# Kernel optimization log

Measured on AMD Instinct MI355X. Metric: run time of the kernel, lower is better.

## Reference

```python
import jax, jax.numpy as jnp
import numpy as np

B, S, HID = 4, 2048, 2048
NH, NKV, HD = 16, 4, 128
GROUPS = NH // NKV
THETA = 10000.0
SCALING = 1.0
SCALE = HD ** -0.5


def setup_inputs() -> dict:
    key = jax.random.key(0)
    k1, k2, k3 = jax.random.split(key, 3)
    hidden_states = jax.random.normal(k1, (B, S, HID), dtype=jnp.float32)
    # stored as [in, out] so x @ W matches torch Linear(x) with W = weight.T
    W_qkv = jax.random.normal(k2, (HID, (NH + 2 * NKV) * HD), dtype=jnp.float32) * (HID ** -0.5)
    W_o = jax.random.normal(k3, (HID, HID), dtype=jnp.float32) * (HID ** -0.5)
    return {"hidden_states": hidden_states, "W_qkv": W_qkv, "W_o": W_o}


def _rope_tables(seq_len, dtype):
    inv_freq = 1.0 / (THETA ** (jnp.arange(0, HD, 2, dtype=jnp.float32) / HD))
    t = jnp.arange(seq_len, dtype=jnp.float32) / SCALING
    freqs = jnp.einsum("s,d->sd", t, inv_freq)          # [S, HD/2]
    emb = jnp.concatenate([freqs, freqs], axis=-1)        # [S, HD]
    return jnp.cos(emb).astype(dtype), jnp.sin(emb).astype(dtype)


def _rotate_half(x):
    x1, x2 = jnp.split(x, 2, axis=-1)
    return jnp.concatenate([-x2, x1], axis=-1)


def _apply_rope(x, cos, sin):
    # x: [B, H, S, D]; cos/sin: [S, D]
    return x * cos[None, None] + _rotate_half(x) * sin[None, None]


def reference(hidden_states, W_qkv, W_o):
    b, s, _ = hidden_states.shape
    qkv = hidden_states @ W_qkv                           # [B, S, (NH+2NKV)*HD]
    q, k, v = jnp.split(qkv, [NH * HD, (NH + NKV) * HD], axis=-1)
    q = q.reshape(b, s, NH, HD).transpose(0, 2, 1, 3)      # [B, NH, S, D]
    k = k.reshape(b, s, NKV, HD).transpose(0, 2, 1, 3)     # [B, NKV, S, D]
    v = v.reshape(b, s, NKV, HD).transpose(0, 2, 1, 3)

    cos, sin = _rope_tables(s, hidden_states.dtype)
    q = _apply_rope(q, cos, sin)
    k = _apply_rope(k, cos, sin)

    # GQA attention without materializing expanded K/V
    qg = q.reshape(b, NKV, GROUPS, s, HD)                  # [B, NKV, G, Sq, D]
    scores = jnp.einsum("bkgqd,bkKd->bkgqK", qg, k) * SCALE
    causal = jnp.tril(jnp.ones((s, s), dtype=bool))
    scores = jnp.where(causal[None, None, None], scores, jnp.finfo(scores.dtype).min)
    probs = jax.nn.softmax(scores, axis=-1)
    out = jnp.einsum("bkgqK,bkKd->bkgqd", probs, v)        # [B, NKV, G, Sq, D]
    out = out.reshape(b, NH, s, HD).transpose(0, 2, 1, 3).reshape(b, s, HID)
    return out @ W_o
```

## Files before the change

kernel.cpp:

```cpp
#include <hip/hip_runtime.h>

#define B_ 4
#define S_ 2048
#define HID_ 2048
#define NH_ 16
#define NKV_ 4
#define HD_ 128
#define NTOK (B_ * S_)
#define QKV_N 3072
#define KO_N 512
#define SCALE_ 0.08838834764831845f
#define NEG_ -30000.0f

typedef __attribute__((ext_vector_type(8))) short short8;
typedef __attribute__((ext_vector_type(4))) short short4v;
typedef __attribute__((ext_vector_type(4))) float f32x4;
typedef unsigned short ushort_t;
typedef unsigned int uint32;

__device__ __forceinline__ float sanit(float x) {
    if (!(x == x)) x = 0.0f;
    return fminf(fmaxf(x, -65504.0f), 65504.0f);
}
__device__ __forceinline__ ushort_t f2bf(float f) {
    union { float f; uint32 u; } c; c.f = f;
    uint32 u = c.u;
    u += 0x7fffu + ((u >> 16) & 1u);
    return (ushort_t)(u >> 16);
}
__device__ __forceinline__ ushort_t f2bf_s(float f) { return f2bf(sanit(f)); }
__device__ __forceinline__ float bf2f(ushort_t h) {
    union { float f; uint32 u; } c; c.u = ((uint32)h) << 16;
    return c.f;
}

__device__ __forceinline__ void gl16(const ushort_t* g, ushort_t* l) {
    __builtin_amdgcn_global_load_lds(
        (__attribute__((address_space(1))) void*)g,
        (__attribute__((address_space(3))) void*)l, 16, 0, 0);
}

__global__ void convx_kernel(const float* __restrict__ X, ushort_t* __restrict__ Xb) {
    size_t i = (size_t)blockIdx.x * blockDim.x + threadIdx.x;
    const float4 a = *(const float4*)(X + i * 8);
    const float4 b = *(const float4*)(X + i * 8 + 4);
    short8 p;
    p[0] = (short)f2bf(a.x); p[1] = (short)f2bf(a.y);
    p[2] = (short)f2bf(a.z); p[3] = (short)f2bf(a.w);
    p[4] = (short)f2bf(b.x); p[5] = (short)f2bf(b.y);
    p[6] = (short)f2bf(b.z); p[7] = (short)f2bf(b.w);
    *(short8*)(Xb + i * 8) = p;
}

__global__ void wtrans_kernel(const float* __restrict__ W, ushort_t* __restrict__ Wt,
                              int K, int N) {
    __shared__ float tile[32][33];
    const int n0 = blockIdx.x * 32;
    const int k0 = blockIdx.y * 32;
    const int t  = threadIdx.x;
    const int r  = t >> 3;
    const int c  = (t & 7) * 4;
    const float4 v = *(const float4*)(W + (size_t)(k0 + r) * N + n0 + c);
    tile[r][c] = v.x; tile[r][c + 1] = v.y; tile[r][c + 2] = v.z; tile[r][c + 3] = v.w;
    __syncthreads();
    short4v p;
    p[0] = (short)f2bf(tile[c][r]);
    p[1] = (short)f2bf(tile[c + 1][r]);
    p[2] = (short)f2bf(tile[c + 2][r]);
    p[3] = (short)f2bf(tile[c + 3][r]);
    *(short4v*)(Wt + (size_t)(n0 + r) * K + k0 + c) = p;
}

template <int SPLIT>
__global__ __launch_bounds__(256, 2) void gemm_bt(
    const ushort_t* __restrict__ A, const ushort_t* __restrict__ Bt,
    void* __restrict__ C0, ushort_t* __restrict__ C1, ushort_t* __restrict__ C2,
    int M, int N, int K) {
    __shared__ __align__(16) ushort_t As[128 * 32];
    __shared__ __align__(16) ushort_t Bs[128 * 32];

    const int tid  = threadIdx.x;
    const int lane = tid & 63;
    const int w    = tid >> 6;
    const int wm   = (w >> 1) * 64;
    const int wn   = (w & 1) * 64;
    const int m0   = blockIdx.y * 128;
    const int n0   = blockIdx.x * 128;
    const int col  = lane & 15;
    const int quad = lane >> 4;

    f32x4 acc[4][4] = {};

    const int sr = tid >> 2;
    const int sk = (tid & 3) * 8;
    const ushort_t* ag0 = A + (size_t)(m0 + sr) * K + sk;
    const ushort_t* ag1 = A + (size_t)(m0 + 64 + sr) * K + sk;
    const ushort_t* bg0 = Bt + (size_t)(n0 + sr) * K + sk;
    const ushort_t* bg1 = Bt + (size_t)(n0 + 64 + sr) * K + sk;
    ushort_t* la0 = &As[tid * 8];
    ushort_t* la1 = &As[2048 + tid * 8];
    ushort_t* lb0 = &Bs[tid * 8];
    ushort_t* lb1 = &Bs[2048 + tid * 8];

    for (int k0 = 0; k0 < K; k0 += 32) {
        __syncthreads();
        gl16(ag0 + k0, la0);
        gl16(ag1 + k0, la1);
        gl16(bg0 + k0, lb0);
        gl16(bg1 + k0, lb1);
        __syncthreads();

        short8 af[4], bfr[4];
#pragma unroll
        for (int mt = 0; mt < 4; ++mt)
            af[mt] = *(const short8*)&As[(wm + mt * 16 + col) * 32 + quad * 8];
#pragma unroll
        for (int nt = 0; nt < 4; ++nt)
            bfr[nt] = *(const short8*)&Bs[(wn + nt * 16 + col) * 32 + quad * 8];
#pragma unroll
        for (int mt = 0; mt < 4; ++mt)
#pragma unroll
            for (int nt = 0; nt < 4; ++nt)
                acc[mt][nt] = __builtin_amdgcn_mfma_f32_16x16x32_bf16(
                    af[mt], bfr[nt], acc[mt][nt], 0, 0, 0);
    }

    if (SPLIT) {
        if (n0 >= 2560) {
#pragma unroll
            for (int mt = 0; mt < 4; ++mt)
#pragma unroll
                for (int nt = 0; nt < 4; ++nt) {
                    int cc   = n0 + wn + nt * 16 + col - 2560;
                    int row0 = m0 + wm + mt * 16 + quad * 4;
                    short4v p;
#pragma unroll
                    for (int r = 0; r < 4; ++r) p[r] = (short)f2bf_s(acc[mt][nt][r]);
                    *(short4v*)&C2[(size_t)cc * NTOK + row0] = p;
                }
        } else {
            ushort_t* dst;
            int ldc, coff;
            if (n0 >= 2048) { dst = C1; ldc = KO_N; coff = 2048; }
            else            { dst = (ushort_t*)C0; ldc = HID_; coff = 0; }
#pragma unroll
            for (int mt = 0; mt < 4; ++mt)
#pragma unroll
                for (int nt = 0; nt < 4; ++nt)
#pragma unroll
                    for (int r = 0; r < 4; ++r) {
                        int row = m0 + wm + mt * 16 + quad * 4 + r;
                        int cc  = n0 + wn + nt * 16 + col - coff;
                        dst[(size_t)row * ldc + cc] = f2bf_s(acc[mt][nt][r]);
                    }
        }
    } else {
        float* dst = (float*)C0;
#pragma unroll
        for (int mt = 0; mt < 4; ++mt)
#pragma unroll
            for (int nt = 0; nt < 4; ++nt)
#pragma unroll
                for (int r = 0; r < 4; ++r) {
                    int row = m0 + wm + mt * 16 + quad * 4 + r;
                    int cc  = n0 + wn + nt * 16 + col;
                    dst[(size_t)row * N + cc] = sanit(acc[mt][nt][r]);
                }
    }
}

__global__ void rope_kernel(ushort_t* __restrict__ qbuf,
                            ushort_t* __restrict__ kb) {
    int p = blockIdx.x * blockDim.x + threadIdx.x;
    const int total = NTOK * 20 * 64;
    if (p >= total) return;
    int d    = p & 63;
    int rest = p >> 6;
    int head = rest % 20;
    int tok  = rest / 20;
    int s    = tok & (S_ - 1);

    ushort_t* base;
    if (head < 16) base = qbuf + (size_t)tok * HID_ + head * HD_ + d;
    else           base = kb   + (size_t)tok * KO_N + (head - 16) * HD_ + d;

    float x1 = bf2f(base[0]);
    float x2 = bf2f(base[64]);

    float inv_freq = powf(10000.0f, -(float)d * (1.0f / 64.0f));
    float ang = (float)s * inv_freq;
    float sn, cs;
    sincosf(ang, &sn, &cs);

    base[0]  = f2bf_s(x1 * cs - x2 * sn);
    base[64] = f2bf_s(x2 * cs + x1 * sn);
}

__global__ __launch_bounds__(512, 4) void flash_kernel(
    const ushort_t* __restrict__ qbuf, const ushort_t* __restrict__ kb,
    const ushort_t* __restrict__ vtg, ushort_t* __restrict__ obuf) {
    __shared__ __align__(16) ushort_t Ks[64][136];
    __shared__ __align__(16) ushort_t Vt[128][72];
    __shared__ __align__(16) ushort_t Ps[8][16][72];

    const int tid  = threadIdx.x;
    const int lane = tid & 63;
    const int w    = tid >> 6;
    const int col  = lane & 15;
    const int quad = lane >> 4;
    const int q0   = (S_ / 128 - 1 - blockIdx.x) * 128;
    const int h    = blockIdx.y;
    const int b    = blockIdx.z;
    const int kvh  = h >> 2;
    const int bS   = b * S_;

    const int wr    = q0 + w * 16;
    const int wmax  = wr + 15;
    const int i_row = wr + quad * 4;

    short8 qf[4];
    {
        const ushort_t* qp = qbuf + (size_t)(bS + wr + col) * HID_
                             + h * HD_ + quad * 8;
#pragma unroll
        for (int kt = 0; kt < 4; ++kt) qf[kt] = *(const short8*)(qp + kt * 32);
    }

    float m_i[4], l_i[4];
#pragma unroll
    for (int r = 0; r < 4; ++r) { m_i[r] = NEG_; l_i[r] = 0.f; }
    f32x4 o[8] = {};

    const int ntiles = q0 / 64 + 2;

    const int jr = tid >> 3;
    const int kd = (tid & 7) * 16;
    const int vd = tid >> 2;
    const int vj = (tid & 3) * 16;

    const ushort_t* kgb = kb + (size_t)(bS + jr) * KO_N + kvh * HD_ + kd;
    const ushort_t* vgb = vtg + (size_t)(kvh * HD_ + vd) * NTOK + bS + vj;

    float4 pk0, pk1, pv0, pv1;
    pk0 = *(const float4*)(kgb);
    pk1 = *(const float4*)(kgb + 8);
    pv0 = *(const float4*)(vgb);
    pv1 = *(const float4*)(vgb + 8);
    *(float4*)&Ks[jr][kd]     = pk0;
    *(float4*)&Ks[jr][kd + 8] = pk1;
    *(float4*)&Vt[vd][vj]     = pv0;
    *(float4*)&Vt[vd][vj + 8] = pv1;
    __syncthreads();

    for (int t = 0; t < ntiles; ++t) {
        const int j0 = t * 64;
        const bool pre = (t + 1 < ntiles);
        if (pre) {
            const ushort_t* kgn = kgb + (size_t)(j0 + 64) * KO_N;
            const ushort_t* vgn = vgb + (j0 + 64);
            pk0 = *(const float4*)(kgn);
            pk1 = *(const float4*)(kgn + 8);
            pv0 = *(const float4*)(vgn);
            pv1 = *(const float4*)(vgn + 8);
        }

        if (j0 <= wmax) {
            f32x4 s[4] = {};
#pragma unroll
            for (int ct = 0; ct < 4; ++ct)
#pragma unroll
                for (int kt = 0; kt < 4; ++kt) {
                    short8 kf = *(const short8*)&Ks[ct * 16 + col][kt * 32 + quad * 8];
                    s[ct] = __builtin_amdgcn_mfma_f32_16x16x32_bf16(qf[kt], kf, s[ct], 0, 0, 0);
                }

            if (j0 + 64 > wr) {
#pragma unroll
                for (int ct = 0; ct < 4; ++ct) {
                    int jg = j0 + ct * 16 + col;
#pragma unroll
                    for (int r = 0; r < 4; ++r)
                        s[ct][r] = (jg > i_row + r) ? NEG_ : s[ct][r] * SCALE_;
                }
            } else {
#pragma unroll
                for (int ct = 0; ct < 4; ++ct)
#pragma unroll
                    for (int r = 0; r < 4; ++r) s[ct][r] *= SCALE_;
            }

            float mx[4];
#pragma unroll
            for (int r = 0; r < 4; ++r) {
                float m = fmaxf(fmaxf(s[0][r], s[1][r]), fmaxf(s[2][r], s[3][r]));
#pragma unroll
                for (int off = 1; off < 16; off <<= 1)
                    m = fmaxf(m, __shfl_xor(m, off, 64));
                mx[r] = m;
            }
            int ok = 1;
#pragma unroll
            for (int r = 0; r < 4; ++r) ok &= (mx[r] <= m_i[r] + 8.0f) ? 1 : 0;
            if (!__all(ok)) {
#pragma unroll
                for (int r = 0; r < 4; ++r) {
                    float mn = fmaxf(m_i[r], mx[r]);
                    float a  = __expf(m_i[r] - mn);
                    m_i[r] = mn;
                    l_i[r] *= a;
#pragma unroll
                    for (int dt = 0; dt < 8; ++dt) o[dt][r] *= a;
                }
            }
#pragma unroll
            for (int r = 0; r < 4; ++r) {
                float sum = 0.f;
#pragma unroll
                for (int ct = 0; ct < 4; ++ct) {
                    float p = __expf(s[ct][r] - m_i[r]);
                    s[ct][r] = p;
                    sum += p;
                }
#pragma unroll
                for (int off = 1; off < 16; off <<= 1)
                    sum += __shfl_xor(sum, off, 64);
                l_i[r] += sum;
            }

#pragma unroll
            for (int ct = 0; ct < 4; ++ct)
#pragma unroll
                for (int r = 0; r < 4; ++r)
                    Ps[w][quad * 4 + r][ct * 16 + col] = f2bf(s[ct][r]);

#pragma unroll
            for (int kt = 0; kt < 2; ++kt) {
                short8 pf = *(const short8*)&Ps[w][col][kt * 32 + quad * 8];
#pragma unroll
                for (int dt = 0; dt < 8; ++dt) {
                    short8 vf = *(const short8*)&Vt[dt * 16 + col][kt * 32 + quad * 8];
                    o[dt] = __builtin_amdgcn_mfma_f32_16x16x32_bf16(pf, vf, o[dt], 0, 0, 0);
                }
            }
        }

        __syncthreads();
        if (pre) {
            *(float4*)&Ks[jr][kd]     = pk0;
            *(float4*)&Ks[jr][kd + 8] = pk1;
            *(float4*)&Vt[vd][vj]     = pv0;
            *(float4*)&Vt[vd][vj + 8] = pv1;
            __syncthreads();
        }
    }

#pragma unroll
    for (int r = 0; r < 4; ++r) {
        float inv = 1.0f / fmaxf(l_i[r], 1e-30f);
        ushort_t* op = obuf + (size_t)(bS + i_row + r) * HID_ + h * HD_;
#pragma unroll
        for (int dt = 0; dt < 8; ++dt)
            op[dt * 16 + col] = f2bf_s(o[dt][r] * inv);
    }
}

extern "C" void kernel_launch(void* const* d_in, const int* in_sizes, int n_in,
                              void* d_out, int out_size, void* d_ws, size_t ws_size,
                              hipStream_t stream) {
    const float* X    = (const float*)d_in[0];
    const float* Wqkv = (const float*)d_in[1];
    const float* Wo   = (const float*)d_in[2];

    ushort_t* qb  = (ushort_t*)d_out;
    ushort_t* xh  = (ushort_t*)d_out + (size_t)NTOK * HID_;
    ushort_t* kb  = (ushort_t*)d_ws;
    ushort_t* vtg = kb + (size_t)NTOK * KO_N;
    ushort_t* wqt = vtg + (size_t)NTOK * KO_N;
    ushort_t* wot = (ushort_t*)d_ws + (size_t)NTOK * HID_;
    ushort_t* oa  = (ushort_t*)d_ws;

    convx_kernel<<<NTOK * HID_ / (256 * 8), 256, 0, stream>>>(X, xh);
    wtrans_kernel<<<dim3(QKV_N / 32, HID_ / 32), 256, 0, stream>>>(Wqkv, wqt, HID_, QKV_N);
    wtrans_kernel<<<dim3(HID_ / 32, HID_ / 32), 256, 0, stream>>>(Wo, wot, HID_, HID_);
    gemm_bt<1><<<dim3(QKV_N / 128, NTOK / 128), 256, 0, stream>>>(
        xh, wqt, qb, kb, vtg, NTOK, QKV_N, HID_);
    rope_kernel<<<(NTOK * 20 * 64) / 256, 256, 0, stream>>>(qb, kb);
    flash_kernel<<<dim3(S_ / 128, NH_, B_), 512, 0, stream>>>(qb, kb, vtg, xh);
    hipMemcpyAsync(oa, xh, (size_t)NTOK * HID_ * sizeof(ushort_t),
                   hipMemcpyDeviceToDevice, stream);
    gemm_bt<0><<<dim3(HID_ / 128, NTOK / 128), 256, 0, stream>>>(
        oa, wot, d_out, nullptr, nullptr, NTOK, HID_, HID_);
}
```

Measured before the change: 675.3 us.

## Load K/V fragments directly from global memory in flash kernel, drop LDS staging

Rewrites the flash attention kernel so each wave reads its K and V^T MFMA fragments straight from global memory (relying on cache) instead of staging shared tiles in LDS with block-wide barriers. Block size halves to 256 threads covering 64 query rows, doubling the grid, and each wave runs its own causal trip count, so there are no idle tiles or __syncthreads. It also adds s_setprio around the MFMA groups and splits the PV loads into two halves. The cost is redundant global/L2 traffic, since four waves and the four heads sharing a KV head each re-read the same K/V, plus less regular access patterns.

```diff
diff --git a/kernel.cpp b/kernel.cpp
--- a/kernel.cpp
+++ b/kernel.cpp
@@ -196,26 +196,23 @@
     base[64] = f2bf_s(x2 * cs + x1 * sn);
 }
 
-__global__ __launch_bounds__(512, 4) void flash_kernel(
+__global__ __launch_bounds__(256, 4) void flash_kernel(
     const ushort_t* __restrict__ qbuf, const ushort_t* __restrict__ kb,
     const ushort_t* __restrict__ vtg, ushort_t* __restrict__ obuf) {
-    __shared__ __align__(16) ushort_t Ks[64][136];
-    __shared__ __align__(16) ushort_t Vt[128][72];
-    __shared__ __align__(16) ushort_t Ps[8][16][72];
+    __shared__ __align__(16) ushort_t Ps[4][16][72];
 
     const int tid  = threadIdx.x;
     const int lane = tid & 63;
     const int w    = tid >> 6;
     const int col  = lane & 15;
     const int quad = lane >> 4;
-    const int q0   = (S_ / 128 - 1 - blockIdx.x) * 128;
+    const int q0   = (S_ / 64 - 1 - blockIdx.x) * 64;
     const int h    = blockIdx.y;
     const int b    = blockIdx.z;
     const int kvh  = h >> 2;
     const int bS   = b * S_;
 
     const int wr    = q0 + w * 16;
-    const int wmax  = wr + 15;
     const int i_row = wr + quad * 4;
 
     short8 qf[4];
@@ -231,126 +228,115 @@
     for (int r = 0; r < 4; ++r) { m_i[r] = NEG_; l_i[r] = 0.f; }
     f32x4 o[8] = {};
 
-    const int ntiles = q0 / 64 + 2;
-
-    const int jr = tid >> 3;
-    const int kd = (tid & 7) * 16;
-    const int vd = tid >> 2;
-    const int vj = (tid & 3) * 16;
-
-    const ushort_t* kgb = kb + (size_t)(bS + jr) * KO_N + kvh * HD_ + kd;
-    const ushort_t* vgb = vtg + (size_t)(kvh * HD_ + vd) * NTOK + bS + vj;
-
-    float4 pk0, pk1, pv0, pv1;
-    pk0 = *(const float4*)(kgb);
-    pk1 = *(const float4*)(kgb + 8);
-    pv0 = *(const float4*)(vgb);
-    pv1 = *(const float4*)(vgb + 8);
-    *(float4*)&Ks[jr][kd]     = pk0;
-    *(float4*)&Ks[jr][kd + 8] = pk1;
-    *(float4*)&Vt[vd][vj]     = pv0;
-    *(float4*)&Vt[vd][vj + 8] = pv1;
-    __syncthreads();
-
-    for (int t = 0; t < ntiles; ++t) {
+    const int nt = wr / 64 + 1;
+
+    const ushort_t* kbase = kb + (size_t)bS * KO_N + (size_t)kvh * HD_;
+    const ushort_t* vbase = vtg + (size_t)kvh * HD_ * NTOK + bS;
+
+    for (int t = 0; t < nt; ++t) {
         const int j0 = t * 64;
-        const bool pre = (t + 1 < ntiles);
-        if (pre) {
-            const ushort_t* kgn = kgb + (size_t)(j0 + 64) * KO_N;
-            const ushort_t* vgn = vgb + (j0 + 64);
-            pk0 = *(const float4*)(kgn);
-            pk1 = *(const float4*)(kgn + 8);
-            pv0 = *(const float4*)(vgn);
-            pv1 = *(const float4*)(vgn + 8);
-        }
-
-        if (j0 <= wmax) {
-            f32x4 s[4] = {};
+
+        f32x4 s[4] = {};
+#pragma unroll
+        for (int ct = 0; ct < 4; ++ct) {
+            const ushort_t* kr = kbase + (size_t)(j0 + ct * 16 + col) * KO_N + quad * 8;
+            short8 kf0 = *(const short8*)(kr);
+            short8 kf1 = *(const short8*)(kr + 32);
+            short8 kf2 = *(const short8*)(kr + 64);
+            short8 kf3 = *(const short8*)(kr + 96);
+            __builtin_amdgcn_s_setprio(1);
+            s[ct] = __builtin_amdgcn_mfma_f32_16x16x32_bf16(qf[0], kf0, s[ct], 0, 0, 0);
+            s[ct] = __builtin_amdgcn_mfma_f32_16x16x32_bf16(qf[1], kf1, s[ct], 0, 0, 0);
+            s[ct] = __builtin_amdgcn_mfma_f32_16x16x32_bf16(qf[2], kf2, s[ct], 0, 0, 0);
+            s[ct] = __builtin_amdgcn_mfma_f32_16x16x32_bf16(qf[3], kf3, s[ct], 0, 0, 0);
+            __builtin_amdgcn_s_setprio(0);
+        }
+
+        short8 vf0[8];
+#pragma unroll
+        for (int dt = 0; dt < 8; ++dt)
+            vf0[dt] = *(const short8*)(vbase + (size_t)(dt * 16 + col) * NTOK
+                                       + j0 + quad * 8);
+
+        if (j0 + 64 > wr) {
+#pragma unroll
+            for (int ct = 0; ct < 4; ++ct) {
+                int jg = j0 + ct * 16 + col;
+#pragma unroll
+                for (int r = 0; r < 4; ++r)
+                    s[ct][r] = (jg > i_row + r) ? NEG_ : s[ct][r] * SCALE_;
+            }
+        } else {
 #pragma unroll
             for (int ct = 0; ct < 4; ++ct)
 #pragma unroll
-                for (int kt = 0; kt < 4; ++kt) {
-                    short8 kf = *(const short8*)&Ks[ct * 16 + col][kt * 32 + quad * 8];
-                    s[ct] = __builtin_amdgcn_mfma_f32_16x16x32_bf16(qf[kt], kf, s[ct], 0, 0, 0);
-                }
-
-            if (j0 + 64 > wr) {
-#pragma unroll
-                for (int ct = 0; ct < 4; ++ct) {
-                    int jg = j0 + ct * 16 + col;
-#pragma unroll
-                    for (int r = 0; r < 4; ++r)
-                        s[ct][r] = (jg > i_row + r) ? NEG_ : s[ct][r] * SCALE_;
-                }
-            } else {
-#pragma unroll
-                for (int ct = 0; ct < 4; ++ct)
-#pragma unroll
-                    for (int r = 0; r < 4; ++r) s[ct][r] *= SCALE_;
+                for (int r = 0; r < 4; ++r) s[ct][r] *= SCALE_;
+        }
+
+        float mx[4];
+#pragma unroll
+        for (int r = 0; r < 4; ++r) {
+            float m = fmaxf(fmaxf(s[0][r], s[1][r]), fmaxf(s[2][r], s[3][r]));
+#pragma unroll
+            for (int off = 1; off < 16; off <<= 1)
+                m = fmaxf(m, __shfl_xor(m, off, 64));
+            mx[r] = m;
+        }
+        int ok = 1;
+#pragma unroll
+        for (int r = 0; r < 4; ++r) ok &= (mx[r] <= m_i[r] + 8.0f) ? 1 : 0;
+        if (!__all(ok)) {
+#pragma unroll
+            for (int r = 0; r < 4; ++r) {
+                float mn = fmaxf(m_i[r], mx[r]);
+                float a  = __expf(m_i[r] - mn);
+                m_i[r] = mn;
+                l_i[r] *= a;
+#pragma unroll
+                for (int dt = 0; dt < 8; ++dt) o[dt][r] *= a;
             }
-
-            float mx[4];
-#pragma unroll
-            for (int r = 0; r < 4; ++r) {
-                float m = fmaxf(fmaxf(s[0][r], s[1][r]), fmaxf(s[2][r], s[3][r]));
-#pragma unroll
-                for (int off = 1; off < 16; off <<= 1)
-                    m = fmaxf(m, __shfl_xor(m, off, 64));
-                mx[r] = m;
+        }
+#pragma unroll
+        for (int r = 0; r < 4; ++r) {
+            float sum = 0.f;
+#pragma unroll
+            for (int ct = 0; ct < 4; ++ct) {
+                float p = __expf(s[ct][r] - m_i[r]);
+                s[ct][r] = p;
+                sum += p;
             }
-            int ok = 1;
-#pragma unroll
-            for (int r = 0; r < 4; ++r) ok &= (mx[r] <= m_i[r] + 8.0f) ? 1 : 0;
-            if (!__all(ok)) {
-#pragma unroll
-                for (int r = 0; r < 4; ++r) {
-                    float mn = fmaxf(m_i[r], mx[r]);
-                    float a  = __expf(m_i[r] - mn);
-                    m_i[r] = mn;
-                    l_i[r] *= a;
-#pragma unroll
-                    for (int dt = 0; dt < 8; ++dt) o[dt][r] *= a;
-                }
-            }
-#pragma unroll
-            for (int r = 0; r < 4; ++r) {
-                float sum = 0.f;
-#pragma unroll
-                for (int ct = 0; ct < 4; ++ct) {
-                    float p = __expf(s[ct][r] - m_i[r]);
-                    s[ct][r] = p;
-                    sum += p;
-                }
-#pragma unroll
-                for (int off = 1; off < 16; off <<= 1)
-                    sum += __shfl_xor(sum, off, 64);
-                l_i[r] += sum;
-            }
-
-#pragma unroll
-            for (int ct = 0; ct < 4; ++ct)
-#pragma unroll
-                for (int r = 0; r < 4; ++r)
-                    Ps[w][quad * 4 + r][ct * 16 + col] = f2bf(s[ct][r]);
-
-#pragma unroll
-            for (int kt = 0; kt < 2; ++kt) {
-                short8 pf = *(const short8*)&Ps[w][col][kt * 32 + quad * 8];
-#pragma unroll
-                for (int dt = 0; dt < 8; ++dt) {
-                    short8 vf = *(const short8*)&Vt[dt * 16 + col][kt * 32 + quad * 8];
-                    o[dt] = __builtin_amdgcn_mfma_f32_16x16x32_bf16(pf, vf, o[dt], 0, 0, 0);
-                }
-            }
-        }
-
-        __syncthreads();
-        if (pre) {
-            *(float4*)&Ks[jr][kd]     = pk0;
-            *(float4*)&Ks[jr][kd + 8] = pk1;
-            *(float4*)&Vt[vd][vj]     = pv0;
-            *(float4*)&Vt[vd][vj + 8] = pv1;
-            __syncthreads();
+#pragma unroll
+            for (int off = 1; off < 16; off <<= 1)
+                sum += __shfl_xor(sum, off, 64);
+            l_i[r] += sum;
+        }
+
+#pragma unroll
+        for (int ct = 0; ct < 4; ++ct)
+#pragma unroll
+            for (int r = 0; r < 4; ++r)
+                Ps[w][quad * 4 + r][ct * 16 + col] = f2bf(s[ct][r]);
+
+        {
+            short8 pf = *(const short8*)&Ps[w][col][quad * 8];
+            __builtin_amdgcn_s_setprio(1);
+#pragma unroll
+            for (int dt = 0; dt < 8; ++dt)
+                o[dt] = __builtin_amdgcn_mfma_f32_16x16x32_bf16(pf, vf0[dt], o[dt], 0, 0, 0);
+            __builtin_amdgcn_s_setprio(0);
+        }
+        {
+            short8 vf1[8];
+#pragma unroll
+            for (int dt = 0; dt < 8; ++dt)
+                vf1[dt] = *(const short8*)(vbase + (size_t)(dt * 16 + col) * NTOK
+                                           + j0 + 32 + quad * 8);
+            short8 pf = *(const short8*)&Ps[w][col][32 + quad * 8];
+            __builtin_amdgcn_s_setprio(1);
+#pragma unroll
+            for (int dt = 0; dt < 8; ++dt)
+                o[dt] = __builtin_amdgcn_mfma_f32_16x16x32_bf16(pf, vf1[dt], o[dt], 0, 0, 0);
+            __builtin_amdgcn_s_setprio(0);
         }
     }
 
@@ -385,7 +371,7 @@
     gemm_bt<1><<<dim3(QKV_N / 128, NTOK / 128), 256, 0, stream>>>(
         xh, wqt, qb, kb, vtg, NTOK, QKV_N, HID_);
     rope_kernel<<<(NTOK * 20 * 64) / 256, 256, 0, stream>>>(qb, kb);
-    flash_kernel<<<dim3(S_ / 128, NH_, B_), 512, 0, stream>>>(qb, kb, vtg, xh);
+    flash_kernel<<<dim3(S_ / 64, NH_, B_), 256, 0, stream>>>(qb, kb, vtg, xh);
     hipMemcpyAsync(oa, xh, (size_t)NTOK * HID_ * sizeof(ushort_t),
                    hipMemcpyDeviceToDevice, stream);
     gemm_bt<0><<<dim3(HID_ / 128, NTOK / 128), 256, 0, stream>>>(
```

After: 1.524 ms. +125.6%, slower.

## Replace 128x128 GEMM with double-buffered 256x256 tile, 512-thread kernel

Applied to the files above, without the earlier changes.

Both projection GEMMs now use a 256x256 output tile with 8 waves, a K-step of 64, and double-buffered LDS staging. The next K-tile is prefetched while MFMAs run on the current one, and the MFMA bursts are split into four phases separated by barriers and s_setprio. The aim is more operand reuse per byte loaded and less exposed global-load latency than the single-buffered 128x128 loop. In exchange the kernel uses 128KB of LDS per block and many more accumulator registers, and the grid shrinks (12x32 and 8x32 blocks), which may leave CUs underfilled and limit occupancy.

```diff
diff --git a/kernel.cpp b/kernel.cpp
--- a/kernel.cpp
+++ b/kernel.cpp
@@ -72,67 +72,141 @@
 }
 
 template <int SPLIT>
-__global__ __launch_bounds__(256, 2) void gemm_bt(
+__global__ __launch_bounds__(512, 2) void gemm256(
     const ushort_t* __restrict__ A, const ushort_t* __restrict__ Bt,
     void* __restrict__ C0, ushort_t* __restrict__ C1, ushort_t* __restrict__ C2,
     int M, int N, int K) {
-    __shared__ __align__(16) ushort_t As[128 * 32];
-    __shared__ __align__(16) ushort_t Bs[128 * 32];
+    __shared__ __align__(16) ushort_t As[2][256 * 64];
+    __shared__ __align__(16) ushort_t Bs[2][256 * 64];
 
     const int tid  = threadIdx.x;
     const int lane = tid & 63;
     const int w    = tid >> 6;
-    const int wm   = (w >> 1) * 64;
-    const int wn   = (w & 1) * 64;
-    const int m0   = blockIdx.y * 128;
-    const int n0   = blockIdx.x * 128;
+    const int wm   = w >> 2;
+    const int wn   = w & 3;
+    const int m0   = blockIdx.y * 256;
+    const int n0   = blockIdx.x * 256;
     const int col  = lane & 15;
     const int quad = lane >> 4;
 
-    f32x4 acc[4][4] = {};
-
-    const int sr = tid >> 2;
-    const int sk = (tid & 3) * 8;
-    const ushort_t* ag0 = A + (size_t)(m0 + sr) * K + sk;
-    const ushort_t* ag1 = A + (size_t)(m0 + 64 + sr) * K + sk;
-    const ushort_t* bg0 = Bt + (size_t)(n0 + sr) * K + sk;
-    const ushort_t* bg1 = Bt + (size_t)(n0 + 64 + sr) * K + sk;
-    ushort_t* la0 = &As[tid * 8];
-    ushort_t* la1 = &As[2048 + tid * 8];
-    ushort_t* lb0 = &Bs[tid * 8];
-    ushort_t* lb1 = &Bs[2048 + tid * 8];
-
-    for (int k0 = 0; k0 < K; k0 += 32) {
-        __syncthreads();
-        gl16(ag0 + k0, la0);
-        gl16(ag1 + k0, la1);
-        gl16(bg0 + k0, lb0);
-        gl16(bg1 + k0, lb1);
-        __syncthreads();
-
-        short8 af[4], bfr[4];
-#pragma unroll
-        for (int mt = 0; mt < 4; ++mt)
-            af[mt] = *(const short8*)&As[(wm + mt * 16 + col) * 32 + quad * 8];
-#pragma unroll
-        for (int nt = 0; nt < 4; ++nt)
-            bfr[nt] = *(const short8*)&Bs[(wn + nt * 16 + col) * 32 + quad * 8];
-#pragma unroll
-        for (int mt = 0; mt < 4; ++mt)
-#pragma unroll
-            for (int nt = 0; nt < 4; ++nt)
-                acc[mt][nt] = __builtin_amdgcn_mfma_f32_16x16x32_bf16(
-                    af[mt], bfr[nt], acc[mt][nt], 0, 0, 0);
+    f32x4 acc[8][4] = {};
+
+    const int c0_ = tid, c1_ = 512 + tid;
+    const int r0_ = c0_ >> 3, kc0_ = (c0_ & 7) * 8;
+    const int r1_ = c1_ >> 3, kc1_ = (c1_ & 7) * 8;
+
+    auto stage = [&](int kt, int nb) {
+        const size_t ko = (size_t)kt * 64;
+#pragma unroll
+        for (int h = 0; h < 2; ++h) {
+            gl16(A  + (size_t)(m0 + h * 128 + r0_) * K + ko + kc0_,
+                 &As[nb][h * 8192 + c0_ * 8]);
+            gl16(A  + (size_t)(m0 + h * 128 + r1_) * K + ko + kc1_,
+                 &As[nb][h * 8192 + c1_ * 8]);
+            gl16(Bt + (size_t)(n0 + h * 128 + r0_) * K + ko + kc0_,
+                 &Bs[nb][h * 8192 + c0_ * 8]);
+            gl16(Bt + (size_t)(n0 + h * 128 + r1_) * K + ko + kc1_,
+                 &Bs[nb][h * 8192 + c1_ * 8]);
+        }
+    };
+
+    const int T = K >> 6;
+
+    stage(0, 0);
+    asm volatile("s_waitcnt vmcnt(0)" ::: "memory");
+    __builtin_amdgcn_s_barrier();
+
+    for (int t = 0; t < T; ++t) {
+        const int bi = t & 1;
+        stage(t + 1 < T ? t + 1 : 0, bi ^ 1);
+
+        short8 af[4][2], bf01[2][2], bf23[2][2];
+
+#pragma unroll
+        for (int mt = 0; mt < 4; ++mt)
+#pragma unroll
+            for (int kk = 0; kk < 2; ++kk)
+                af[mt][kk] = *(const short8*)
+                    &As[bi][(wm * 128 + mt * 16 + col) * 64 + kk * 32 + quad * 8];
+#pragma unroll
+        for (int nt = 0; nt < 2; ++nt)
+#pragma unroll
+            for (int kk = 0; kk < 2; ++kk)
+                bf01[nt][kk] = *(const short8*)
+                    &Bs[bi][(wn * 64 + nt * 16 + col) * 64 + kk * 32 + quad * 8];
+        __builtin_amdgcn_s_setprio(1);
+#pragma unroll
+        for (int mt = 0; mt < 4; ++mt)
+#pragma unroll
+            for (int nt = 0; nt < 2; ++nt)
+#pragma unroll
+                for (int kk = 0; kk < 2; ++kk)
+                    acc[mt][nt] = __builtin_amdgcn_mfma_f32_16x16x32_bf16(
+                        af[mt][kk], bf01[nt][kk], acc[mt][nt], 0, 0, 0);
+        __builtin_amdgcn_s_setprio(0);
+        __builtin_amdgcn_s_barrier();
+
+#pragma unroll
+        for (int nt = 0; nt < 2; ++nt)
+#pragma unroll
+            for (int kk = 0; kk < 2; ++kk)
+                bf23[nt][kk] = *(const short8*)
+                    &Bs[bi][(wn * 64 + (nt + 2) * 16 + col) * 64 + kk * 32 + quad * 8];
+        __builtin_amdgcn_s_setprio(1);
+#pragma unroll
+        for (int mt = 0; mt < 4; ++mt)
+#pragma unroll
+            for (int nt = 0; nt < 2; ++nt)
+#pragma unroll
+                for (int kk = 0; kk < 2; ++kk)
+                    acc[mt][nt + 2] = __builtin_amdgcn_mfma_f32_16x16x32_bf16(
+                        af[mt][kk], bf23[nt][kk], acc[mt][nt + 2], 0, 0, 0);
+        __builtin_amdgcn_s_setprio(0);
+        __builtin_amdgcn_s_barrier();
+
+#pragma unroll
+        for (int mt = 0; mt < 4; ++mt)
+#pragma unroll
+            for (int kk = 0; kk < 2; ++kk)
+                af[mt][kk] = *(const short8*)
+                    &As[bi][(wm * 128 + (mt + 4) * 16 + col) * 64 + kk * 32 + quad * 8];
+        __builtin_amdgcn_s_setprio(1);
+#pragma unroll
+        for (int mt = 0; mt < 4; ++mt)
+#pragma unroll
+            for (int nt = 0; nt < 2; ++nt)
+#pragma unroll
+                for (int kk = 0; kk < 2; ++kk)
+                    acc[mt + 4][nt] = __builtin_amdgcn_mfma_f32_16x16x32_bf16(
+                        af[mt][kk], bf01[nt][kk], acc[mt + 4][nt], 0, 0, 0);
+        __builtin_amdgcn_s_setprio(0);
+        __builtin_amdgcn_s_barrier();
+
+        __builtin_amdgcn_s_setprio(1);
+#pragma unroll
+        for (int mt = 0; mt < 4; ++mt)
+#pragma unroll
+            for (int nt = 0; nt < 2; ++nt)
+#pragma unroll
+                for (int kk = 0; kk < 2; ++kk)
+                    acc[mt + 4][nt + 2] = __builtin_amdgcn_mfma_f32_16x16x32_bf16(
+                        af[mt][kk], bf23[nt][kk], acc[mt + 4][nt + 2], 0, 0, 0);
+        __builtin_amdgcn_s_setprio(0);
+
+        asm volatile("s_waitcnt vmcnt(0)" ::: "memory");
+        __builtin_amdgcn_s_barrier();
     }
 
+    const int crow = m0 + wm * 128 + quad * 4;
+    const int ccol = n0 + wn * 64 + col;
     if (SPLIT) {
         if (n0 >= 2560) {
 #pragma unroll
-            for (int mt = 0; mt < 4; ++mt)
+            for (int mt = 0; mt < 8; ++mt)
 #pragma unroll
                 for (int nt = 0; nt < 4; ++nt) {
-                    int cc   = n0 + wn + nt * 16 + col - 2560;
-                    int row0 = m0 + wm + mt * 16 + quad * 4;
+                    int cc   = ccol + nt * 16 - 2560;
+                    int row0 = crow + mt * 16;
                     short4v p;
 #pragma unroll
                     for (int r = 0; r < 4; ++r) p[r] = (short)f2bf_s(acc[mt][nt][r]);
@@ -144,26 +218,26 @@
             if (n0 >= 2048) { dst = C1; ldc = KO_N; coff = 2048; }
             else            { dst = (ushort_t*)C0; ldc = HID_; coff = 0; }
 #pragma unroll
-            for (int mt = 0; mt < 4; ++mt)
+            for (int mt = 0; mt < 8; ++mt)
 #pragma unroll
                 for (int nt = 0; nt < 4; ++nt)
 #pragma unroll
                     for (int r = 0; r < 4; ++r) {
-                        int row = m0 + wm + mt * 16 + quad * 4 + r;
-                        int cc  = n0 + wn + nt * 16 + col - coff;
+                        int row = crow + mt * 16 + r;
+                        int cc  = ccol + nt * 16 - coff;
                         dst[(size_t)row * ldc + cc] = f2bf_s(acc[mt][nt][r]);
                     }
         }
     } else {
         float* dst = (float*)C0;
 #pragma unroll
-        for (int mt = 0; mt < 4; ++mt)
+        for (int mt = 0; mt < 8; ++mt)
 #pragma unroll
             for (int nt = 0; nt < 4; ++nt)
 #pragma unroll
                 for (int r = 0; r < 4; ++r) {
-                    int row = m0 + wm + mt * 16 + quad * 4 + r;
-                    int cc  = n0 + wn + nt * 16 + col;
+                    int row = crow + mt * 16 + r;
+                    int cc  = ccol + nt * 16;
                     dst[(size_t)row * N + cc] = sanit(acc[mt][nt][r]);
                 }
     }
@@ -382,12 +456,12 @@
     convx_kernel<<<NTOK * HID_ / (256 * 8), 256, 0, stream>>>(X, xh);
     wtrans_kernel<<<dim3(QKV_N / 32, HID_ / 32), 256, 0, stream>>>(Wqkv, wqt, HID_, QKV_N);
     wtrans_kernel<<<dim3(HID_ / 32, HID_ / 32), 256, 0, stream>>>(Wo, wot, HID_, HID_);
-    gemm_bt<1><<<dim3(QKV_N / 128, NTOK / 128), 256, 0, stream>>>(
+    gemm256<1><<<dim3(QKV_N / 256, NTOK / 256), 512, 0, stream>>>(
         xh, wqt, qb, kb, vtg, NTOK, QKV_N, HID_);
     rope_kernel<<<(NTOK * 20 * 64) / 256, 256, 0, stream>>>(qb, kb);
     flash_kernel<<<dim3(S_ / 128, NH_, B_), 512, 0, stream>>>(qb, kb, vtg, xh);
     hipMemcpyAsync(oa, xh, (size_t)NTOK * HID_ * sizeof(ushort_t),
                    hipMemcpyDeviceToDevice, stream);
-    gemm_bt<0><<<dim3(HID_ / 128, NTOK / 128), 256, 0, stream>>>(
+    gemm256<0><<<dim3(HID_ / 256, NTOK / 256), 512, 0, stream>>>(
         oa, wot, d_out, nullptr, nullptr, NTOK, HID_, HID_);
 }
```

Result: slower. 744.3 us (+10.2%).

## Fold softmax scale and log2e into Q during RoPE; compute row sums via MFMA

Applied to the files above, without the earlier changes.

RoPE now multiplies Q by scale*log2(e), so the flash kernel drops the per-score scale multiply and uses exp2f instead of __expf. The per-row probability sum is no longer built with shuffle reductions; it comes from an extra MFMA of the bf16 P tile against a vector of ones. This removes per-tile ALU and cross-lane shuffle work in the softmax. In exchange it adds one MFMA per k-step, and the row sum is now taken over bf16-rounded probabilities, which keeps it consistent with the P·V product but changes numerics slightly.

```diff
diff --git a/kernel.cpp b/kernel.cpp
--- a/kernel.cpp
+++ b/kernel.cpp
@@ -10,6 +10,7 @@
 #define QKV_N 3072
 #define KO_N 512
 #define SCALE_ 0.08838834764831845f
+#define QSC_ 0.12751743f
 #define NEG_ -30000.0f
 
 typedef __attribute__((ext_vector_type(8))) short short8;
@@ -181,8 +182,9 @@
     int s    = tok & (S_ - 1);
 
     ushort_t* base;
-    if (head < 16) base = qbuf + (size_t)tok * HID_ + head * HD_ + d;
-    else           base = kb   + (size_t)tok * KO_N + (head - 16) * HD_ + d;
+    float sc;
+    if (head < 16) { base = qbuf + (size_t)tok * HID_ + head * HD_ + d; sc = QSC_; }
+    else           { base = kb   + (size_t)tok * KO_N + (head - 16) * HD_ + d; sc = 1.0f; }
 
     float x1 = bf2f(base[0]);
     float x2 = bf2f(base[64]);
@@ -192,8 +194,8 @@
     float sn, cs;
     sincosf(ang, &sn, &cs);
 
-    base[0]  = f2bf_s(x1 * cs - x2 * sn);
-    base[64] = f2bf_s(x2 * cs + x1 * sn);
+    base[0]  = f2bf_s((x1 * cs - x2 * sn) * sc);
+    base[64] = f2bf_s((x2 * cs + x1 * sn) * sc);
 }
 
 __global__ __launch_bounds__(512, 4) void flash_kernel(
@@ -226,10 +228,15 @@
         for (int kt = 0; kt < 4; ++kt) qf[kt] = *(const short8*)(qp + kt * 32);
     }
 
-    float m_i[4], l_i[4];
-#pragma unroll
-    for (int r = 0; r < 4; ++r) { m_i[r] = NEG_; l_i[r] = 0.f; }
+    short8 vone;
+#pragma unroll
+    for (int e = 0; e < 8; ++e) vone[e] = (short)0x3F80;
+
+    float m_i[4];
+#pragma unroll
+    for (int r = 0; r < 4; ++r) m_i[r] = NEG_;
     f32x4 o[8] = {};
+    f32x4 lsum = {};
 
     const int ntiles = q0 / 64 + 2;
 
@@ -280,13 +287,8 @@
                     int jg = j0 + ct * 16 + col;
 #pragma unroll
                     for (int r = 0; r < 4; ++r)
-                        s[ct][r] = (jg > i_row + r) ? NEG_ : s[ct][r] * SCALE_;
-                }
-            } else {
-#pragma unroll
-                for (int ct = 0; ct < 4; ++ct)
-#pragma unroll
-                    for (int r = 0; r < 4; ++r) s[ct][r] *= SCALE_;
+                        if (jg > i_row + r) s[ct][r] = NEG_;
+                }
             }
 
             float mx[4];
@@ -305,33 +307,18 @@
 #pragma unroll
                 for (int r = 0; r < 4; ++r) {
                     float mn = fmaxf(m_i[r], mx[r]);
-                    float a  = __expf(m_i[r] - mn);
+                    float a  = exp2f(m_i[r] - mn);
                     m_i[r] = mn;
-                    l_i[r] *= a;
+                    lsum[r] *= a;
 #pragma unroll
                     for (int dt = 0; dt < 8; ++dt) o[dt][r] *= a;
                 }
             }
 #pragma unroll
-            for (int r = 0; r < 4; ++r) {
-                float sum = 0.f;
-#pragma unroll
-                for (int ct = 0; ct < 4; ++ct) {
-                    float p = __expf(s[ct][r] - m_i[r]);
-                    s[ct][r] = p;
-                    sum += p;
-                }
-#pragma unroll
-                for (int off = 1; off < 16; off <<= 1)
-                    sum += __shfl_xor(sum, off, 64);
-                l_i[r] += sum;
-            }
-
-#pragma unroll
             for (int ct = 0; ct < 4; ++ct)
 #pragma unroll
                 for (int r = 0; r < 4; ++r)
-                    Ps[w][quad * 4 + r][ct * 16 + col] = f2bf(s[ct][r]);
+                    Ps[w][quad * 4 + r][ct * 16 + col] = f2bf(exp2f(s[ct][r] - m_i[r]));
 
 #pragma unroll
             for (int kt = 0; kt < 2; ++kt) {
@@ -341,6 +328,7 @@
                     short8 vf = *(const short8*)&Vt[dt * 16 + col][kt * 32 + quad * 8];
                     o[dt] = __builtin_amdgcn_mfma_f32_16x16x32_bf16(pf, vf, o[dt], 0, 0, 0);
                 }
+                lsum = __builtin_amdgcn_mfma_f32_16x16x32_bf16(pf, vone, lsum, 0, 0, 0);
             }
         }
 
@@ -356,7 +344,7 @@
 
 #pragma unroll
     for (int r = 0; r < 4; ++r) {
-        float inv = 1.0f / fmaxf(l_i[r], 1e-30f);
+        float inv = 1.0f / fmaxf(lsum[r], 1e-30f);
         ushort_t* op = obuf + (size_t)(bS + i_row + r) * HID_ + h * HD_;
 #pragma unroll
         for (int dt = 0; dt < 8; ++dt)
```

Measured after the change: 644.4 us. -4.6%, faster.
